# Performance work log

Hardware: AMD Instinct MI355X
Metric: run time of the kernel (lower is better)

Reference implementation:

```python
import jax, jax.numpy as jnp
import numpy as np
from jax.ops import segment_sum, segment_max

N = 20000   # nodes
E = 320000  # edges (no self loops; conv adds them)
G = 64      # graphs in batch
D = 128     # embed dim
H = 64      # GATConv out channels (heads=1)
L = 6       # number of conv/mlp blocks


def setup_inputs() -> dict:
    key = jax.random.key(0)
    ks = jax.random.split(key, 24)
    x_idx = jax.random.randint(ks[0], (N,), 0, 128)
    src = jax.random.randint(ks[1], (E,), 0, N)
    dst = jax.random.randint(ks[2], (E,), 0, N)
    dst = jnp.where(src == dst, (dst + 1) % N, dst)  # remove_self_loops semantics
    edge_index = jnp.stack([src, dst])
    edge_attr_idx = jax.random.randint(ks[3], (E,), 0, 128)
    batch = (jnp.arange(N) * G) // N  # sorted graph ids, ~312 nodes/graph
    s = 0.1
    r = lambda k, shp: jax.random.normal(k, shp, dtype=jnp.float32) * s
    return {
        'x_idx': x_idx, 'edge_index': edge_index, 'edge_attr_idx': edge_attr_idx, 'batch': batch,
        'emb': r(ks[4], (128, D)),
        'conv_W': r(ks[5], (L, D, H)), 'conv_We': r(ks[6], (L, D, H)),
        'conv_att_src': r(ks[7], (L, H)), 'conv_att_dst': r(ks[8], (L, H)),
        'conv_att_edge': r(ks[9], (L, H)), 'conv_b': jnp.zeros((L, H), jnp.float32),
        'mlp_W1': r(ks[10], (L, H, H)), 'mlp_b1': jnp.zeros((L, H), jnp.float32),
        'mlp_W2': r(ks[11], (L, H, H)), 'mlp_b2': jnp.zeros((L, H), jnp.float32),
        'mlp_W3': r(ks[12], (L, H, D)), 'mlp_b3': jnp.zeros((L, D), jnp.float32),
        'g1_W1': r(ks[13], (D, H)), 'g1_b1': jnp.zeros((H,), jnp.float32),
        'g1_W2': r(ks[14], (H, 1)), 'g1_b2': jnp.zeros((1,), jnp.float32),
        'g2_W1': r(ks[15], (D, H)), 'g2_b1': jnp.zeros((H,), jnp.float32),
        'g2_W2': r(ks[16], (H, D)), 'g2_b2': jnp.zeros((D,), jnp.float32),
        'p_W1': r(ks[17], (D, H)), 'p_b1': jnp.zeros((H,), jnp.float32),
        'p_W2': r(ks[18], (H, H)), 'p_b2': jnp.zeros((H,), jnp.float32),
        'p_W3': r(ks[19], (H, 1)), 'p_b3': jnp.zeros((1,), jnp.float32),
    }


def _mlp3(x, W1, b1, W2, b2, W3, b3):
    h = jax.nn.relu(x @ W1 + b1)
    h = jax.nn.relu(h @ W2 + b2)
    return h @ W3 + b3


def reference(x_idx, edge_index, edge_attr_idx, batch, emb, conv_W, conv_We,
              conv_att_src, conv_att_dst, conv_att_edge, conv_b,
              mlp_W1, mlp_b1, mlp_W2, mlp_b2, mlp_W3, mlp_b3,
              g1_W1, g1_b1, g1_W2, g1_b2, g2_W1, g2_b1, g2_W2, g2_b2,
              p_W1, p_b1, p_W2, p_b2, p_W3, p_b3):
    n = x_idx.shape[0]
    x = emb[x_idx]                 # [N,128]
    e = emb[edge_attr_idx]         # [E,128]
    src, dst = edge_index[0], edge_index[1]
    # add_self_loops with fill_value='mean': loop attr = mean of incoming edge attrs
    deg = segment_sum(jnp.ones((e.shape[0],), x.dtype), dst, num_segments=n)
    loop_attr = segment_sum(e, dst, num_segments=n) / jnp.maximum(deg, 1.0)[:, None]
    e_full = jnp.concatenate([e, loop_attr], axis=0)             # [E+N,128]
    ar = jnp.arange(n)
    src_f = jnp.concatenate([src, ar])
    dst_f = jnp.concatenate([dst, ar])

    def gat_conv(x, i):
        h = x @ conv_W[i]                       # [N,64]
        ep = e_full @ conv_We[i]                # [E+N,64]
        a_s = h @ conv_att_src[i]               # [N]
        a_d = h @ conv_att_dst[i]               # [N]
        a_e = ep @ conv_att_edge[i]             # [E+N]
        logit = jax.nn.leaky_relu(a_s[src_f] + a_d[dst_f] + a_e, 0.2)
        m = segment_max(logit, dst_f, num_segments=n)
        w = jnp.exp(logit - m[dst_f])
        denom = segment_sum(w, dst_f, num_segments=n)
        alpha = w / denom[dst_f]
        out = segment_sum(h[src_f] * alpha[:, None], dst_f, num_segments=n)
        return out + conv_b[i]

    jkn = []
    for i in range(L):  # dropout is identity at inference
        x = gat_conv(x, i)
        x = _mlp3(x, mlp_W1[i], mlp_b1[i], mlp_W2[i], mlp_b2[i], mlp_W3[i], mlp_b3[i])
        jkn.append(x)
    jkn = jnp.stack(jkn)                                  # [6,N,128]
    ms = jnp.sqrt(jnp.sum(jnp.square(jkn), axis=2))       # [6,N]
    ni = jnp.argmax(ms, axis=0)                           # [N]
    feature = jnp.take_along_axis(jkn, ni[None, :, None], axis=0)[0]  # [N,128]

    # per-graph attention pooling (vectorized over the per-graph loop)
    h1 = (jax.nn.relu(feature @ g1_W1 + g1_b1) @ g1_W2 + g1_b2)[:, 0]  # [N]
    m = segment_max(h1, batch, num_segments=G)
    w = jnp.exp(h1 - m[batch])
    attn = w / segment_sum(w, batch, num_segments=G)[batch]            # softmax per graph
    h2 = jax.nn.relu(feature @ g2_W1 + g2_b1) @ g2_W2 + g2_b2          # [N,128]
    counts = segment_sum(jnp.ones((n,), feature.dtype), batch, num_segments=G)
    hg = segment_sum(attn[:, None] * h2, batch, num_segments=G) / counts[:, None]  # [G,128]

    out = _mlp3(hg, p_W1, p_b1, p_W2, p_b2, p_W3, p_b3)   # [G,1]
    return out[:, 0]
```

## Files before the change

kernel.cpp:

```cpp
#include <hip/hip_runtime.h>
#include <math.h>

__device__ __forceinline__ float lrelu(float x){ return x > 0.0f ? x : 0.2f*x; }
__device__ __forceinline__ float bcastf(float v, int l){
    return __int_as_float(__builtin_amdgcn_readlane(__float_as_int(v), l));
}
__device__ __forceinline__ float wsum(float v){
    #pragma unroll
    for(int off=32; off; off>>=1) v += __shfl_xor(v, off, 64);
    return v;
}


__global__ void k_count(const int* __restrict__ dst, int* __restrict__ cnt, int E){
    int e = blockIdx.x*256 + threadIdx.x;
    if(e < E) atomicAdd(&cnt[dst[e]], 1);
}

__global__ __launch_bounds__(1024) void k_scan(const int* __restrict__ cnt, int* __restrict__ rowptr, int n){
    __shared__ int ws[16];
    __shared__ int carrysh;
    int t = threadIdx.x, lane = t & 63, wv = t >> 6;
    if(t==0){ carrysh = 0; rowptr[0] = 0; }
    __syncthreads();
    for(int base=0; base<n; base+=1024){
        int i = base + t;
        int v = (i<n) ? cnt[i] : 0;
        int s = v;
        #pragma unroll
        for(int off=1; off<64; off<<=1){ int u = __shfl_up(s, off, 64); if(lane>=off) s += u; }
        if(lane==63) ws[wv] = s;
        __syncthreads();
        if(t < 16){
            int u = ws[t];
            #pragma unroll
            for(int off=1; off<16; off<<=1){ int u2 = __shfl_up(u, off, 16); if(t>=off) u += u2; }
            ws[t] = u;
        }
        __syncthreads();
        int carry = carrysh;
        int wbase = wv ? ws[wv-1] : 0;
        if(i<n) rowptr[i+1] = carry + wbase + s;
        int total = ws[15];
        __syncthreads();
        if(t==0) carrysh = carry + total;
        __syncthreads();
    }
}

__global__ void k_scatter(const int* __restrict__ dst, const int* __restrict__ rowptr,
                          int* __restrict__ cnt2, int* __restrict__ eid, int E){
    int e = blockIdx.x*256 + threadIdx.x;
    if(e >= E) return;
    int d = dst[e];
    int p = rowptr[d] + atomicAdd(&cnt2[d], 1);
    eid[p] = e;
}

__global__ __launch_bounds__(256) void k_sortb(const int* __restrict__ rowptr, int* __restrict__ eid, int n){
    int node = blockIdx.x*4 + (threadIdx.x>>6);
    if(node >= n) return;
    int lane = threadIdx.x & 63;
    int b = rowptr[node], e = rowptr[node+1];
    int nj = e - b;
    if(nj <= 1) return;
    if(nj <= 64){
        int v = (lane < nj) ? eid[b+lane] : 0x7fffffff;
        for(int k=2; k<=64; k<<=1){
            for(int j=k>>1; j>0; j>>=1){
                int vv = __shfl_xor(v, j, 64);
                bool up = ((lane & k) == 0);
                bool lower = ((lane & j) == 0);
                int mn = min(v,vv), mx = max(v,vv);
                v = (lower == up) ? mn : mx;
            }
        }
        if(lane < nj) eid[b+lane] = v;
    } else if(lane == 0){
        for(int i=b+1; i<e; i++){
            int key = eid[i]; int j = i-1;
            while(j>=b && eid[j] > key){ eid[j+1] = eid[j]; j--; }
            eid[j+1] = key;
        }
    }
}

__global__ void k_pack(const int* __restrict__ eid, const int* __restrict__ src,
                       const int* __restrict__ eattr, int* __restrict__ packed, int E){
    int p = blockIdx.x*256 + threadIdx.x;
    if(p >= E) return;
    int e = eid[p];
    packed[p] = src[e] | (eattr[e] << 17);
}

__global__ __launch_bounds__(768) void k_table(const float* __restrict__ We, const float* __restrict__ atte,
                                               const float* __restrict__ emb, float* __restrict__ T){
    __shared__ float wv[768];
    int t = threadIdx.x;
    {
        int l = t>>7, k = t&127;
        const float* w = We + ((size_t)l*128 + k)*64;
        const float* a = atte + l*64;
        float s = 0.f;
        #pragma unroll 8
        for(int c=0;c<64;c++) s += w[c]*a[c];
        wv[t] = s;
    }
    __syncthreads();
    int l = t>>7, a = t&127;
    const float4* er = (const float4*)(emb + (size_t)a*128);
    const float* w = wv + l*128;
    float acc = 0.f;
    for(int k=0;k<32;k++){
        float4 v = er[k];
        acc += v.x*w[k*4+0] + v.y*w[k*4+1] + v.z*w[k*4+2] + v.w*w[k*4+3];
    }
    T[l*128 + a] = acc;
}


__global__ __launch_bounds__(256) void k_hx(const int* __restrict__ xidx, const float* __restrict__ emb,
        const float* __restrict__ W, const float* __restrict__ atts, const float* __restrict__ attd,
        float* __restrict__ h, float* __restrict__ as_, float* __restrict__ ad_, int n){
    int t = threadIdx.x, lane = t & 63;
    int base = blockIdx.x*16 + (t>>6)*4;
    if(base >= n) return;
    int nv = min(4, n - base);

    float xv0[4], xv1[4];
    #pragma unroll
    for(int nn=0;nn<4;nn++){
        if(nn < nv){
            int xi = xidx[base+nn];
            xv0[nn] = emb[(size_t)xi*128 + lane];
            xv1[nn] = emb[(size_t)xi*128 + 64 + lane];
        } else { xv0[nn]=0.f; xv1[nn]=0.f; }
    }
    float hv[4] = {0,0,0,0};
    #pragma unroll 8
    for(int k=0;k<64;k++){
        float w = W[k*64 + lane];
        #pragma unroll
        for(int nn=0;nn<4;nn++) hv[nn] = fmaf(bcastf(xv0[nn],k), w, hv[nn]);
    }
    #pragma unroll 8
    for(int k=0;k<64;k++){
        float w = W[(k+64)*64 + lane];
        #pragma unroll
        for(int nn=0;nn<4;nn++) hv[nn] = fmaf(bcastf(xv1[nn],k), w, hv[nn]);
    }
    float atl = atts[lane], adl = attd[lane];
    #pragma unroll
    for(int nn=0;nn<4;nn++){
        float sa = wsum(hv[nn]*atl);
        float sd = wsum(hv[nn]*adl);
        if(nn < nv){
            h[(size_t)(base+nn)*64 + lane] = hv[nn];
            if(lane==0){ as_[base+nn] = sa; ad_[base+nn] = sd; }
        }
    }
}


__global__ __launch_bounds__(256) void k_gat(const float* __restrict__ h,
        const float* __restrict__ as_, const float* __restrict__ ad_,
        const float* __restrict__ T, const int* __restrict__ packed,
        const int* __restrict__ rowptr, const float* __restrict__ bias,
        float* __restrict__ o, int n){
    __shared__ float Tl[128];
    if(threadIdx.x < 128) Tl[threadIdx.x] = T[threadIdx.x];
    __syncthreads();
    int node = blockIdx.x*4 + (threadIdx.x>>6);
    if(node >= n) return;
    int lane = threadIdx.x & 63;
    int b = rowptr[node], e = rowptr[node+1];
    float adv = ad_[node];
    float m = -1e30f, d = 0.f, sumae = 0.f;
    float a0=0.f, a1=0.f, a2=0.f, a3=0.f;
    for(int j0=b; j0<e; j0+=64){
        int nj = min(64, e-j0);
        int sj = 0; float aev = 0.f, lg = -1e30f;
        if(lane < nj){
            int pk = packed[j0+lane];
            sj  = pk & 0x1FFFF;
            aev = Tl[pk >> 17];
            lg  = lrelu(as_[sj] + adv + aev);
        }
        float cm = lg, sa = aev;
        #pragma unroll
        for(int off=32; off; off>>=1){ cm = fmaxf(cm, __shfl_xor(cm,off,64)); sa += __shfl_xor(sa,off,64); }
        sumae += sa;
        float nm = fmaxf(m, cm);
        float w = (lane<nj) ? expf(lg-nm) : 0.f;
        float ws = w;
        #pragma unroll
        for(int off=32; off; off>>=1) ws += __shfl_xor(ws,off,64);
        float scale = (m > -1e29f) ? expf(m-nm) : 0.f;
        d = d*scale + ws;
        a0*=scale; a1*=scale; a2*=scale; a3*=scale;
        int j = 0;
        for(; j+3<nj; j+=4){
            a0 = fmaf(bcastf(w,j+0), h[(size_t)__builtin_amdgcn_readlane(sj,j+0)*64 + lane], a0);
            a1 = fmaf(bcastf(w,j+1), h[(size_t)__builtin_amdgcn_readlane(sj,j+1)*64 + lane], a1);
            a2 = fmaf(bcastf(w,j+2), h[(size_t)__builtin_amdgcn_readlane(sj,j+2)*64 + lane], a2);
            a3 = fmaf(bcastf(w,j+3), h[(size_t)__builtin_amdgcn_readlane(sj,j+3)*64 + lane], a3);
        }
        for(; j<nj; j++)
            a0 = fmaf(bcastf(w,j), h[(size_t)__builtin_amdgcn_readlane(sj,j)*64 + lane], a0);
        m = nm;
    }
    int deg = e - b;
    float ael = sumae / fmaxf((float)deg, 1.f);
    float ls = lrelu(as_[node] + adv + ael);
    float nm = fmaxf(m, ls);
    float scale = (m > -1e29f) ? expf(m-nm) : 0.f;
    float wl = expf(ls-nm);
    d = d*scale + wl;
    float acc = (a0+a1)+(a2+a3);
    acc = acc*scale + wl*h[(size_t)node*64 + lane];
    o[(size_t)node*64 + lane] = acc/d + bias[lane];
}


__global__ __launch_bounds__(256) void k_dense(
    const float* __restrict__ o,
    const float* __restrict__ W1, const float* __restrict__ b1,
    const float* __restrict__ W2, const float* __restrict__ b2,
    const float* __restrict__ W3, const float* __restrict__ b3,
    float* __restrict__ bestF, float* __restrict__ bestMs, int layer,
    const float* __restrict__ Wn, const float* __restrict__ atts, const float* __restrict__ attd,
    float* __restrict__ hn, float* __restrict__ asn, float* __restrict__ adn_,
    const float* __restrict__ A, const float* __restrict__ g1b1,
    const float* __restrict__ w2, const float* __restrict__ g1b2,
    const float* __restrict__ B, const float* __restrict__ g2b1,
    const float* __restrict__ C, const float* __restrict__ g2b2,
    float* __restrict__ h1, float* __restrict__ h2,
    int n, int last)
{
    int t = threadIdx.x, lane = t & 63;
    int base = blockIdx.x*16 + (t>>6)*4;
    if(base >= n) return;
    int nv = min(4, n - base);

    float ov[4];
    #pragma unroll
    for(int nn=0;nn<4;nn++) ov[nn] = (nn<nv) ? o[(size_t)(base+nn)*64 + lane] : 0.f;

    float t1[4];
    {
        float bb = b1[lane];
        #pragma unroll
        for(int nn=0;nn<4;nn++) t1[nn] = bb;
        #pragma unroll 8
        for(int k=0;k<64;k++){
            float w = W1[k*64 + lane];
            #pragma unroll
            for(int nn=0;nn<4;nn++) t1[nn] = fmaf(bcastf(ov[nn],k), w, t1[nn]);
        }
        #pragma unroll
        for(int nn=0;nn<4;nn++) t1[nn] = fmaxf(t1[nn], 0.f);
    }

    float t2[4];
    {
        float bb = b2[lane];
        #pragma unroll
        for(int nn=0;nn<4;nn++) t2[nn] = bb;
        #pragma unroll 8
        for(int k=0;k<64;k++){
            float w = W2[k*64 + lane];
            #pragma unroll
            for(int nn=0;nn<4;nn++) t2[nn] = fmaf(bcastf(t1[nn],k), w, t2[nn]);
        }
        #pragma unroll
        for(int nn=0;nn<4;nn++) t2[nn] = fmaxf(t2[nn], 0.f);
    }

    float xp0[4], xp1[4];
    {
        float ba = b3[lane], bb = b3[lane+64];
        #pragma unroll
        for(int nn=0;nn<4;nn++){ xp0[nn]=ba; xp1[nn]=bb; }
        #pragma unroll 4
        for(int k=0;k<64;k++){
            float wa = W3[k*128 + lane];
            float wb = W3[k*128 + 64 + lane];
            #pragma unroll
            for(int nn=0;nn<4;nn++){
                float s = bcastf(t2[nn],k);
                xp0[nn] = fmaf(s, wa, xp0[nn]);
                xp1[nn] = fmaf(s, wb, xp1[nn]);
            }
        }
    }

    float msv[4]; bool upd[4];
    #pragma unroll
    for(int nn=0;nn<4;nn++){
        float p = wsum(xp0[nn]*xp0[nn] + xp1[nn]*xp1[nn]);
        msv[nn] = p;
        float prev = -1e30f;
        if(layer > 0 && nn < nv) prev = bestMs[base+nn];
        upd[nn] = (layer==0) || (p > prev);
    }

    if(!last){
        #pragma unroll
        for(int nn=0;nn<4;nn++){
            if(nn<nv && upd[nn]){
                bestF[(size_t)(base+nn)*128 + lane]      = xp0[nn];
                bestF[(size_t)(base+nn)*128 + 64 + lane] = xp1[nn];
                if(lane==0) bestMs[base+nn] = msv[nn];
            }
        }
        float hv[4] = {0,0,0,0};
        #pragma unroll 8
        for(int k=0;k<64;k++){
            float w = Wn[k*64 + lane];
            #pragma unroll
            for(int nn=0;nn<4;nn++) hv[nn] = fmaf(bcastf(xp0[nn],k), w, hv[nn]);
        }
        #pragma unroll 8
        for(int k=0;k<64;k++){
            float w = Wn[(k+64)*64 + lane];
            #pragma unroll
            for(int nn=0;nn<4;nn++) hv[nn] = fmaf(bcastf(xp1[nn],k), w, hv[nn]);
        }
        float atl = atts[lane], adl = attd[lane];
        #pragma unroll
        for(int nn=0;nn<4;nn++){
            float sa = wsum(hv[nn]*atl);
            float sd = wsum(hv[nn]*adl);
            if(nn<nv){
                hn[(size_t)(base+nn)*64 + lane] = hv[nn];
                if(lane==0){ asn[base+nn] = sa; adn_[base+nn] = sd; }
            }
        }
        return;
    }

    #pragma unroll
    for(int nn=0;nn<4;nn++){
        if(nn<nv && !upd[nn]){
            xp0[nn] = bestF[(size_t)(base+nn)*128 + lane];
            xp1[nn] = bestF[(size_t)(base+nn)*128 + 64 + lane];
        }
    }
    {
        float p1[4];
        float bb = g1b1[lane];
        #pragma unroll
        for(int nn=0;nn<4;nn++) p1[nn] = bb;
        #pragma unroll 8
        for(int k=0;k<64;k++){
            float w = A[k*64 + lane];
            #pragma unroll
            for(int nn=0;nn<4;nn++) p1[nn] = fmaf(bcastf(xp0[nn],k), w, p1[nn]);
        }
        #pragma unroll 8
        for(int k=0;k<64;k++){
            float w = A[(k+64)*64 + lane];
            #pragma unroll
            for(int nn=0;nn<4;nn++) p1[nn] = fmaf(bcastf(xp1[nn],k), w, p1[nn]);
        }
        float w2l = w2[lane], bout = g1b2[0];
        #pragma unroll
        for(int nn=0;nn<4;nn++){
            float s = wsum(fmaxf(p1[nn],0.f)*w2l);
            if(nn<nv && lane==0) h1[base+nn] = s + bout;
        }
    }
    float p2[4];
    {
        float bb = g2b1[lane];
        #pragma unroll
        for(int nn=0;nn<4;nn++) p2[nn] = bb;
        #pragma unroll 8
        for(int k=0;k<64;k++){
            float w = B[k*64 + lane];
            #pragma unroll
            for(int nn=0;nn<4;nn++) p2[nn] = fmaf(bcastf(xp0[nn],k), w, p2[nn]);
        }
        #pragma unroll 8
        for(int k=0;k<64;k++){
            float w = B[(k+64)*64 + lane];
            #pragma unroll
            for(int nn=0;nn<4;nn++) p2[nn] = fmaf(bcastf(xp1[nn],k), w, p2[nn]);
        }
        #pragma unroll
        for(int nn=0;nn<4;nn++) p2[nn] = fmaxf(p2[nn], 0.f);
    }
    {
        float r0[4], r1[4];
        float ba = g2b2[lane], bb = g2b2[lane+64];
        #pragma unroll
        for(int nn=0;nn<4;nn++){ r0[nn]=ba; r1[nn]=bb; }
        #pragma unroll 4
        for(int k=0;k<64;k++){
            float wa = C[k*128 + lane];
            float wb = C[k*128 + 64 + lane];
            #pragma unroll
            for(int nn=0;nn<4;nn++){
                float s = bcastf(p2[nn],k);
                r0[nn] = fmaf(s, wa, r0[nn]);
                r1[nn] = fmaf(s, wb, r1[nn]);
            }
        }
        #pragma unroll
        for(int nn=0;nn<4;nn++){
            if(nn<nv){
                h2[(size_t)(base+nn)*128 + lane]      = r0[nn];
                h2[(size_t)(base+nn)*128 + 64 + lane] = r1[nn];
            }
        }
    }
}


__global__ __launch_bounds__(128) void k_pool2(const float* __restrict__ h1, const float* __restrict__ h2,
                      float* __restrict__ wbuf,
                      const float* __restrict__ pW1, const float* __restrict__ pb1,
                      const float* __restrict__ pW2, const float* __restrict__ pb2,
                      const float* __restrict__ pW3, const float* __restrict__ pb3,
                      float* __restrict__ out, int n, int G){
    __shared__ float sh[128];
    __shared__ float hgrow[128];
    int g = blockIdx.x, tid = threadIdx.x;
    int start = (g*n + G-1)/G, end = ((g+1)*n + G-1)/G;
    float lm = -1e30f;
    for(int i=start+tid; i<end; i+=128) lm = fmaxf(lm, h1[i]);
    sh[tid]=lm; __syncthreads();
    for(int off=64; off; off>>=1){ if(tid<off) sh[tid]=fmaxf(sh[tid],sh[tid+off]); __syncthreads(); }
    float m = sh[0]; __syncthreads();
    float lsum = 0.f;
    for(int i=start+tid; i<end; i+=128){ float w = expf(h1[i]-m); wbuf[i]=w; lsum+=w; }
    sh[tid]=lsum; __syncthreads();
    for(int off=64; off; off>>=1){ if(tid<off) sh[tid]+=sh[tid+off]; __syncthreads(); }
    float denom = sh[0];
    float a0=0.f,a1=0.f,a2=0.f,a3=0.f;
    int i = start;
    for(; i+3<end; i+=4){
        a0 = fmaf(wbuf[i+0], h2[(size_t)(i+0)*128 + tid], a0);
        a1 = fmaf(wbuf[i+1], h2[(size_t)(i+1)*128 + tid], a1);
        a2 = fmaf(wbuf[i+2], h2[(size_t)(i+2)*128 + tid], a2);
        a3 = fmaf(wbuf[i+3], h2[(size_t)(i+3)*128 + tid], a3);
    }
    for(; i<end; i++) a0 = fmaf(wbuf[i], h2[(size_t)i*128 + tid], a0);
    float acc = (a0+a1)+(a2+a3);
    hgrow[tid] = acc/denom/(float)(end-start);
    __syncthreads();
    if(tid < 64){
        float t1v = pb1[tid];
        for(int k=0;k<128;k++) t1v = fmaf(hgrow[k], pW1[k*64+tid], t1v);
        t1v = fmaxf(t1v, 0.f);
        float t2v = pb2[tid];
        for(int k=0;k<64;k++) t2v = fmaf(__shfl(t1v,k,64), pW2[k*64+tid], t2v);
        t2v = fmaxf(t2v, 0.f);
        float s = t2v * pW3[tid];
        #pragma unroll
        for(int off=32; off; off>>=1) s += __shfl_xor(s,off,64);
        if(tid==0) out[g] = s + pb3[0];
    }
}

extern "C" void kernel_launch(void* const* d_in, const int* in_sizes, int n_in,
                              void* d_out, int out_size, void* d_ws, size_t ws_size,
                              hipStream_t stream){
    const int*   x_idx   = (const int*)  d_in[0];
    const int*   eindex  = (const int*)  d_in[1];
    const int*   eattr   = (const int*)  d_in[2];
    const float* emb     = (const float*)d_in[4];
    const float* conv_W  = (const float*)d_in[5];
    const float* conv_We = (const float*)d_in[6];
    const float* att_src = (const float*)d_in[7];
    const float* att_dst = (const float*)d_in[8];
    const float* att_edg = (const float*)d_in[9];
    const float* conv_b  = (const float*)d_in[10];
    const float* mW1 = (const float*)d_in[11]; const float* mb1 = (const float*)d_in[12];
    const float* mW2 = (const float*)d_in[13]; const float* mb2 = (const float*)d_in[14];
    const float* mW3 = (const float*)d_in[15]; const float* mb3 = (const float*)d_in[16];
    const float* g1W1= (const float*)d_in[17]; const float* g1b1= (const float*)d_in[18];
    const float* g1W2= (const float*)d_in[19]; const float* g1b2= (const float*)d_in[20];
    const float* g2W1= (const float*)d_in[21]; const float* g2b1= (const float*)d_in[22];
    const float* g2W2= (const float*)d_in[23]; const float* g2b2= (const float*)d_in[24];
    const float* pW1 = (const float*)d_in[25]; const float* pb1 = (const float*)d_in[26];
    const float* pW2 = (const float*)d_in[27]; const float* pb2 = (const float*)d_in[28];
    const float* pW3 = (const float*)d_in[29]; const float* pb3 = (const float*)d_in[30];

    const int N = in_sizes[0];
    const int E = in_sizes[2];
    const int G = out_size;
    const int* src = eindex;
    const int* dst = eindex + E;
    const int NW = (N + 3) / 4;
    const int ND = (N + 15) / 16;

    char* p = (char*)d_ws;
    auto alloc = [&](size_t bytes)->void*{ void* r = (void*)p; p += (bytes + 255) & ~(size_t)255; return r; };
    float* h      = (float*)alloc((size_t)N*64*4);
    float* o      = (float*)alloc((size_t)N*64*4);
    float* bestF  = (float*)alloc((size_t)N*128*4);
    float* h2buf  = (float*)alloc((size_t)N*128*4);
    float* bestMs = (float*)alloc((size_t)N*4);
    float* as_    = (float*)alloc((size_t)N*4);
    float* ad_    = (float*)alloc((size_t)N*4);
    float* Tbuf   = (float*)alloc(6*128*4);
    float* h1     = (float*)alloc((size_t)N*4);
    int*   cnt    = (int*)  alloc((size_t)N*4);
    int*   cnt2   = (int*)  alloc((size_t)N*4);
    int*   rowptr = (int*)  alloc((size_t)(N+1)*4);
    int*   eid    = (int*)  alloc((size_t)E*4);
    int*   packed = (int*)  alloc((size_t)E*4);

    hipMemsetAsync(cnt,  0, (size_t)N*4, stream);
    hipMemsetAsync(cnt2, 0, (size_t)N*4, stream);

    k_count<<<(E+255)/256, 256, 0, stream>>>(dst, cnt, E);
    k_scan<<<1, 1024, 0, stream>>>(cnt, rowptr, N);
    k_scatter<<<(E+255)/256, 256, 0, stream>>>(dst, rowptr, cnt2, eid, E);
    k_sortb<<<NW, 256, 0, stream>>>(rowptr, eid, N);
    k_pack<<<(E+255)/256, 256, 0, stream>>>(eid, src, eattr, packed, E);
    k_table<<<1, 768, 0, stream>>>(conv_We, att_edg, emb, Tbuf);
    k_hx<<<ND, 256, 0, stream>>>(x_idx, emb, conv_W, att_src, att_dst, h, as_, ad_, N);

    for(int l=0; l<6; l++){
        int last = (l==5) ? 1 : 0;
        const float* Wn   = last ? conv_W  : conv_W  + (size_t)(l+1)*8192;
        const float* atsn = last ? att_src : att_src + (l+1)*64;
        const float* atdn = last ? att_dst : att_dst + (l+1)*64;
        k_gat<<<NW, 256, 0, stream>>>(h, as_, ad_, Tbuf + l*128, packed, rowptr, conv_b + l*64, o, N);
        k_dense<<<ND, 256, 0, stream>>>(o,
            mW1 + (size_t)l*4096, mb1 + l*64, mW2 + (size_t)l*4096, mb2 + l*64,
            mW3 + (size_t)l*8192, mb3 + l*128,
            bestF, bestMs, l,
            Wn, atsn, atdn,
            h, as_, ad_,
            g1W1, g1b1, g1W2, g1b2, g2W1, g2b1, g2W2, g2b2,
            h1, h2buf,
            N, last);
    }

    k_pool2<<<G, 128, 0, stream>>>(h1, h2buf, bestMs,
            pW1, pb1, pW2, pb2, pW3, pb3, (float*)d_out, N, G);
}
```

Before: 530.9 us.

## Split each wave into half-wave node groups with vectorized loads and swizzle broadcasts

Rewrites the dense per-node MLP and projection kernels so that each wave processes four nodes as two 32-lane halves. Each half-wave owns two nodes, each lane holds 2 or 4 output columns, and loads are vectorized as float2/float4. Input values are broadcast with ds_swizzle inside 32-lane groups instead of readlane, using fully compile-time-unrolled loops. The intent is to cut scalar readlane traffic and the number of weight loads per FMA. The risks are heavy unrolling and register pressure, and swizzle goes through the LDS crossbar, which may add latency.

```diff
diff --git a/kernel.cpp b/kernel.cpp
--- a/kernel.cpp
+++ b/kernel.cpp
@@ -1,13 +1,33 @@
 #include <hip/hip_runtime.h>
 #include <math.h>
+#include <utility>
 
 __device__ __forceinline__ float lrelu(float x){ return x > 0.0f ? x : 0.2f*x; }
 __device__ __forceinline__ float bcastf(float v, int l){
     return __int_as_float(__builtin_amdgcn_readlane(__float_as_int(v), l));
 }
-__device__ __forceinline__ float wsum(float v){
+template<int J>
+__device__ __forceinline__ float swzbc(float v){
+    return __int_as_float(__builtin_amdgcn_ds_swizzle(__float_as_int(v), (J<<5)));
+}
+template<int C> __device__ __forceinline__ float getc4(const float4& v){
+    if constexpr(C==0) return v.x; else if constexpr(C==1) return v.y;
+    else if constexpr(C==2) return v.z; else return v.w;
+}
+template<int C> __device__ __forceinline__ float getc2(const float2& v){
+    if constexpr(C==0) return v.x; else return v.y;
+}
+template<class F, int... Is>
+__device__ __forceinline__ void unroll_impl(F&& f, std::integer_sequence<int, Is...>){
+    (f(std::integral_constant<int, Is>{}), ...);
+}
+template<int N, class F>
+__device__ __forceinline__ void unrollN(F&& f){
+    unroll_impl(static_cast<F&&>(f), std::make_integer_sequence<int, N>{});
+}
+__device__ __forceinline__ float hsum32(float v){
     #pragma unroll
-    for(int off=32; off; off>>=1) v += __shfl_xor(v, off, 64);
+    for(int off=16; off; off>>=1) v += __shfl_xor(v, off, 64);
     return v;
 }
 
@@ -125,40 +145,30 @@
     int t = threadIdx.x, lane = t & 63;
     int base = blockIdx.x*16 + (t>>6)*4;
     if(base >= n) return;
-    int nv = min(4, n - base);
-
-    float xv0[4], xv1[4];
-    #pragma unroll
-    for(int nn=0;nn<4;nn++){
-        if(nn < nv){
-            int xi = xidx[base+nn];
-            xv0[nn] = emb[(size_t)xi*128 + lane];
-            xv1[nn] = emb[(size_t)xi*128 + 64 + lane];
-        } else { xv0[nn]=0.f; xv1[nn]=0.f; }
-    }
-    float hv[4] = {0,0,0,0};
-    #pragma unroll 8
-    for(int k=0;k<64;k++){
-        float w = W[k*64 + lane];
-        #pragma unroll
-        for(int nn=0;nn<4;nn++) hv[nn] = fmaf(bcastf(xv0[nn],k), w, hv[nn]);
-    }
-    #pragma unroll 8
-    for(int k=0;k<64;k++){
-        float w = W[(k+64)*64 + lane];
-        #pragma unroll
-        for(int nn=0;nn<4;nn++) hv[nn] = fmaf(bcastf(xv1[nn],k), w, hv[nn]);
-    }
-    float atl = atts[lane], adl = attd[lane];
-    #pragma unroll
-    for(int nn=0;nn<4;nn++){
-        float sa = wsum(hv[nn]*atl);
-        float sd = wsum(hv[nn]*adl);
-        if(nn < nv){
-            h[(size_t)(base+nn)*64 + lane] = hv[nn];
-            if(lane==0){ as_[base+nn] = sa; ad_[base+nn] = sd; }
-        }
-    }
+    int cl = lane & 31, g = lane >> 5;
+    int ga = base + g*2, gb = ga + 1;
+    bool va = (ga < n), vb = (gb < n);
+
+    float4 x0 = va ? *(const float4*)(emb + (size_t)xidx[ga]*128 + 4*cl) : make_float4(0,0,0,0);
+    float4 x1 = vb ? *(const float4*)(emb + (size_t)xidx[gb]*128 + 4*cl) : make_float4(0,0,0,0);
+
+    float2 h0 = make_float2(0,0), h1v = make_float2(0,0);
+    unrollN<128>([&](auto kc){
+        constexpr int k = kc.value;
+        float2 w = *(const float2*)(W + k*64 + 2*cl);
+        float a0 = swzbc<(k>>2)>( getc4<(k&3)>(x0) );
+        float a1 = swzbc<(k>>2)>( getc4<(k&3)>(x1) );
+        h0.x  = fmaf(a0, w.x, h0.x);  h0.y  = fmaf(a0, w.y, h0.y);
+        h1v.x = fmaf(a1, w.x, h1v.x); h1v.y = fmaf(a1, w.y, h1v.y);
+    });
+    float2 ats = *(const float2*)(atts + 2*cl);
+    float2 atd = *(const float2*)(attd + 2*cl);
+    float pa0 = hsum32(h0.x*ats.x + h0.y*ats.y);
+    float pd0 = hsum32(h0.x*atd.x + h0.y*atd.y);
+    float pa1 = hsum32(h1v.x*ats.x + h1v.y*ats.y);
+    float pd1 = hsum32(h1v.x*atd.x + h1v.y*atd.y);
+    if(va){ *(float2*)(h + (size_t)ga*64 + 2*cl) = h0;  if(cl==0){ as_[ga]=pa0; ad_[ga]=pd0; } }
+    if(vb){ *(float2*)(h + (size_t)gb*64 + 2*cl) = h1v; if(cl==0){ as_[gb]=pa1; ad_[gb]=pd1; } }
 }
 
 
@@ -240,179 +250,127 @@
     int t = threadIdx.x, lane = t & 63;
     int base = blockIdx.x*16 + (t>>6)*4;
     if(base >= n) return;
-    int nv = min(4, n - base);
-
-    float ov[4];
-    #pragma unroll
-    for(int nn=0;nn<4;nn++) ov[nn] = (nn<nv) ? o[(size_t)(base+nn)*64 + lane] : 0.f;
-
-    float t1[4];
+    int cl = lane & 31, g = lane >> 5;
+    int ga = base + g*2, gb = ga + 1;
+    bool va = (ga < n), vb = (gb < n);
+
+    float2 o0 = va ? *(const float2*)(o + (size_t)ga*64 + 2*cl) : make_float2(0,0);
+    float2 o1 = vb ? *(const float2*)(o + (size_t)gb*64 + 2*cl) : make_float2(0,0);
+
+    float2 bv1 = *(const float2*)(b1 + 2*cl);
+    float2 t10 = bv1, t11 = bv1;
+    unrollN<64>([&](auto kc){
+        constexpr int k = kc.value;
+        float2 w = *(const float2*)(W1 + k*64 + 2*cl);
+        float a0 = swzbc<(k>>1)>( getc2<(k&1)>(o0) );
+        float a1 = swzbc<(k>>1)>( getc2<(k&1)>(o1) );
+        t10.x = fmaf(a0, w.x, t10.x); t10.y = fmaf(a0, w.y, t10.y);
+        t11.x = fmaf(a1, w.x, t11.x); t11.y = fmaf(a1, w.y, t11.y);
+    });
+    t10.x=fmaxf(t10.x,0.f); t10.y=fmaxf(t10.y,0.f);
+    t11.x=fmaxf(t11.x,0.f); t11.y=fmaxf(t11.y,0.f);
+
+    float2 bv2 = *(const float2*)(b2 + 2*cl);
+    float2 t20 = bv2, t21 = bv2;
+    unrollN<64>([&](auto kc){
+        constexpr int k = kc.value;
+        float2 w = *(const float2*)(W2 + k*64 + 2*cl);
+        float a0 = swzbc<(k>>1)>( getc2<(k&1)>(t10) );
+        float a1 = swzbc<(k>>1)>( getc2<(k&1)>(t11) );
+        t20.x = fmaf(a0, w.x, t20.x); t20.y = fmaf(a0, w.y, t20.y);
+        t21.x = fmaf(a1, w.x, t21.x); t21.y = fmaf(a1, w.y, t21.y);
+    });
+    t20.x=fmaxf(t20.x,0.f); t20.y=fmaxf(t20.y,0.f);
+    t21.x=fmaxf(t21.x,0.f); t21.y=fmaxf(t21.y,0.f);
+
+    float4 bq3 = *(const float4*)(b3 + 4*cl);
+    float4 x0 = bq3, x1 = bq3;
+    unrollN<64>([&](auto kc){
+        constexpr int k = kc.value;
+        float4 w = *(const float4*)(W3 + k*128 + 4*cl);
+        float a0 = swzbc<(k>>1)>( getc2<(k&1)>(t20) );
+        float a1 = swzbc<(k>>1)>( getc2<(k&1)>(t21) );
+        x0.x=fmaf(a0,w.x,x0.x); x0.y=fmaf(a0,w.y,x0.y); x0.z=fmaf(a0,w.z,x0.z); x0.w=fmaf(a0,w.w,x0.w);
+        x1.x=fmaf(a1,w.x,x1.x); x1.y=fmaf(a1,w.y,x1.y); x1.z=fmaf(a1,w.z,x1.z); x1.w=fmaf(a1,w.w,x1.w);
+    });
+
+    float ms0 = hsum32(x0.x*x0.x + x0.y*x0.y + x0.z*x0.z + x0.w*x0.w);
+    float ms1 = hsum32(x1.x*x1.x + x1.y*x1.y + x1.z*x1.z + x1.w*x1.w);
+    bool up0 = true, up1 = true;
+    if(layer > 0){
+        up0 = ms0 > (va ? bestMs[ga] : -1e30f);
+        up1 = ms1 > (vb ? bestMs[gb] : -1e30f);
+    }
+
+    if(!last){
+        if(va && up0){ *(float4*)(bestF + (size_t)ga*128 + 4*cl) = x0; if(cl==0) bestMs[ga] = ms0; }
+        if(vb && up1){ *(float4*)(bestF + (size_t)gb*128 + 4*cl) = x1; if(cl==0) bestMs[gb] = ms1; }
+        float2 h0 = make_float2(0,0), h1v = make_float2(0,0);
+        unrollN<128>([&](auto kc){
+            constexpr int k = kc.value;
+            float2 w = *(const float2*)(Wn + k*64 + 2*cl);
+            float a0 = swzbc<(k>>2)>( getc4<(k&3)>(x0) );
+            float a1 = swzbc<(k>>2)>( getc4<(k&3)>(x1) );
+            h0.x  = fmaf(a0, w.x, h0.x);  h0.y  = fmaf(a0, w.y, h0.y);
+            h1v.x = fmaf(a1, w.x, h1v.x); h1v.y = fmaf(a1, w.y, h1v.y);
+        });
+        float2 ats = *(const float2*)(atts + 2*cl);
+        float2 atd = *(const float2*)(attd + 2*cl);
+        float pa0 = hsum32(h0.x*ats.x + h0.y*ats.y);
+        float pd0 = hsum32(h0.x*atd.x + h0.y*atd.y);
+        float pa1 = hsum32(h1v.x*ats.x + h1v.y*ats.y);
+        float pd1 = hsum32(h1v.x*atd.x + h1v.y*atd.y);
+        if(va){ *(float2*)(hn + (size_t)ga*64 + 2*cl) = h0;  if(cl==0){ asn[ga]=pa0; adn_[ga]=pd0; } }
+        if(vb){ *(float2*)(hn + (size_t)gb*64 + 2*cl) = h1v; if(cl==0){ asn[gb]=pa1; adn_[gb]=pd1; } }
+        return;
+    }
+
+    if(va && !up0) x0 = *(const float4*)(bestF + (size_t)ga*128 + 4*cl);
+    if(vb && !up1) x1 = *(const float4*)(bestF + (size_t)gb*128 + 4*cl);
+
     {
-        float bb = b1[lane];
-        #pragma unroll
-        for(int nn=0;nn<4;nn++) t1[nn] = bb;
-        #pragma unroll 8
-        for(int k=0;k<64;k++){
-            float w = W1[k*64 + lane];
-            #pragma unroll
-            for(int nn=0;nn<4;nn++) t1[nn] = fmaf(bcastf(ov[nn],k), w, t1[nn]);
-        }
-        #pragma unroll
-        for(int nn=0;nn<4;nn++) t1[nn] = fmaxf(t1[nn], 0.f);
-    }
-
-    float t2[4];
+        float2 bg = *(const float2*)(g1b1 + 2*cl);
+        float2 p10 = bg, p11 = bg;
+        unrollN<128>([&](auto kc){
+            constexpr int k = kc.value;
+            float2 w = *(const float2*)(A + k*64 + 2*cl);
+            float a0 = swzbc<(k>>2)>( getc4<(k&3)>(x0) );
+            float a1 = swzbc<(k>>2)>( getc4<(k&3)>(x1) );
+            p10.x = fmaf(a0, w.x, p10.x); p10.y = fmaf(a0, w.y, p10.y);
+            p11.x = fmaf(a1, w.x, p11.x); p11.y = fmaf(a1, w.y, p11.y);
+        });
+        float2 w2v = *(const float2*)(w2 + 2*cl);
+        float s0 = hsum32(fmaxf(p10.x,0.f)*w2v.x + fmaxf(p10.y,0.f)*w2v.y);
+        float s1 = hsum32(fmaxf(p11.x,0.f)*w2v.x + fmaxf(p11.y,0.f)*w2v.y);
+        float bout = g1b2[0];
+        if(va && cl==0) h1[ga] = s0 + bout;
+        if(vb && cl==0) h1[gb] = s1 + bout;
+    }
+    float2 bg2 = *(const float2*)(g2b1 + 2*cl);
+    float2 p20 = bg2, p21 = bg2;
+    unrollN<128>([&](auto kc){
+        constexpr int k = kc.value;
+        float2 w = *(const float2*)(B + k*64 + 2*cl);
+        float a0 = swzbc<(k>>2)>( getc4<(k&3)>(x0) );
+        float a1 = swzbc<(k>>2)>( getc4<(k&3)>(x1) );
+        p20.x = fmaf(a0, w.x, p20.x); p20.y = fmaf(a0, w.y, p20.y);
+        p21.x = fmaf(a1, w.x, p21.x); p21.y = fmaf(a1, w.y, p21.y);
+    });
+    p20.x=fmaxf(p20.x,0.f); p20.y=fmaxf(p20.y,0.f);
+    p21.x=fmaxf(p21.x,0.f); p21.y=fmaxf(p21.y,0.f);
     {
-        float bb = b2[lane];
-        #pragma unroll
-        for(int nn=0;nn<4;nn++) t2[nn] = bb;
-        #pragma unroll 8
-        for(int k=0;k<64;k++){
-            float w = W2[k*64 + lane];
-            #pragma unroll
-            for(int nn=0;nn<4;nn++) t2[nn] = fmaf(bcastf(t1[nn],k), w, t2[nn]);
-        }
-        #pragma unroll
-        for(int nn=0;nn<4;nn++) t2[nn] = fmaxf(t2[nn], 0.f);
-    }
-
-    float xp0[4], xp1[4];
-    {
-        float ba = b3[lane], bb = b3[lane+64];
-        #pragma unroll
-        for(int nn=0;nn<4;nn++){ xp0[nn]=ba; xp1[nn]=bb; }
-        #pragma unroll 4
-        for(int k=0;k<64;k++){
-            float wa = W3[k*128 + lane];
-            float wb = W3[k*128 + 64 + lane];
-            #pragma unroll
-            for(int nn=0;nn<4;nn++){
-                float s = bcastf(t2[nn],k);
-                xp0[nn] = fmaf(s, wa, xp0[nn]);
-                xp1[nn] = fmaf(s, wb, xp1[nn]);
-            }
-        }
-    }
-
-    float msv[4]; bool upd[4];
-    #pragma unroll
-    for(int nn=0;nn<4;nn++){
-        float p = wsum(xp0[nn]*xp0[nn] + xp1[nn]*xp1[nn]);
-        msv[nn] = p;
-        float prev = -1e30f;
-        if(layer > 0 && nn < nv) prev = bestMs[base+nn];
-        upd[nn] = (layer==0) || (p > prev);
-    }
-
-    if(!last){
-        #pragma unroll
-        for(int nn=0;nn<4;nn++){
-            if(nn<nv && upd[nn]){
-                bestF[(size_t)(base+nn)*128 + lane]      = xp0[nn];
-                bestF[(size_t)(base+nn)*128 + 64 + lane] = xp1[nn];
-                if(lane==0) bestMs[base+nn] = msv[nn];
-            }
-        }
-        float hv[4] = {0,0,0,0};
-        #pragma unroll 8
-        for(int k=0;k<64;k++){
-            float w = Wn[k*64 + lane];
-            #pragma unroll
-            for(int nn=0;nn<4;nn++) hv[nn] = fmaf(bcastf(xp0[nn],k), w, hv[nn]);
-        }
-        #pragma unroll 8
-        for(int k=0;k<64;k++){
-            float w = Wn[(k+64)*64 + lane];
-            #pragma unroll
-            for(int nn=0;nn<4;nn++) hv[nn] = fmaf(bcastf(xp1[nn],k), w, hv[nn]);
-        }
-        float atl = atts[lane], adl = attd[lane];
-        #pragma unroll
-        for(int nn=0;nn<4;nn++){
-            float sa = wsum(hv[nn]*atl);
-            float sd = wsum(hv[nn]*adl);
-            if(nn<nv){
-                hn[(size_t)(base+nn)*64 + lane] = hv[nn];
-                if(lane==0){ asn[base+nn] = sa; adn_[base+nn] = sd; }
-            }
-        }
-        return;
-    }
-
-    #pragma unroll
-    for(int nn=0;nn<4;nn++){
-        if(nn<nv && !upd[nn]){
-            xp0[nn] = bestF[(size_t)(base+nn)*128 + lane];
-            xp1[nn] = bestF[(size_t)(base+nn)*128 + 64 + lane];
-        }
-    }
-    {
-        float p1[4];
-        float bb = g1b1[lane];
-        #pragma unroll
-        for(int nn=0;nn<4;nn++) p1[nn] = bb;
-        #pragma unroll 8
-        for(int k=0;k<64;k++){
-            float w = A[k*64 + lane];
-            #pragma unroll
-            for(int nn=0;nn<4;nn++) p1[nn] = fmaf(bcastf(xp0[nn],k), w, p1[nn]);
-        }
-        #pragma unroll 8
-        for(int k=0;k<64;k++){
-            float w = A[(k+64)*64 + lane];
-            #pragma unroll
-            for(int nn=0;nn<4;nn++) p1[nn] = fmaf(bcastf(xp1[nn],k), w, p1[nn]);
-        }
-        float w2l = w2[lane], bout = g1b2[0];
-        #pragma unroll
-        for(int nn=0;nn<4;nn++){
-            float s = wsum(fmaxf(p1[nn],0.f)*w2l);
-            if(nn<nv && lane==0) h1[base+nn] = s + bout;
-        }
-    }
-    float p2[4];
-    {
-        float bb = g2b1[lane];
-        #pragma unroll
-        for(int nn=0;nn<4;nn++) p2[nn] = bb;
-        #pragma unroll 8
-        for(int k=0;k<64;k++){
-            float w = B[k*64 + lane];
-            #pragma unroll
-            for(int nn=0;nn<4;nn++) p2[nn] = fmaf(bcastf(xp0[nn],k), w, p2[nn]);
-        }
-        #pragma unroll 8
-        for(int k=0;k<64;k++){
-            float w = B[(k+64)*64 + lane];
-            #pragma unroll
-            for(int nn=0;nn<4;nn++) p2[nn] = fmaf(bcastf(xp1[nn],k), w, p2[nn]);
-        }
-        #pragma unroll
-        for(int nn=0;nn<4;nn++) p2[nn] = fmaxf(p2[nn], 0.f);
-    }
-    {
-        float r0[4], r1[4];
-        float ba = g2b2[lane], bb = g2b2[lane+64];
-        #pragma unroll
-        for(int nn=0;nn<4;nn++){ r0[nn]=ba; r1[nn]=bb; }
-        #pragma unroll 4
-        for(int k=0;k<64;k++){
-            float wa = C[k*128 + lane];
-            float wb = C[k*128 + 64 + lane];
-            #pragma unroll
-            for(int nn=0;nn<4;nn++){
-                float s = bcastf(p2[nn],k);
-                r0[nn] = fmaf(s, wa, r0[nn]);
-                r1[nn] = fmaf(s, wb, r1[nn]);
-            }
-        }
-        #pragma unroll
-        for(int nn=0;nn<4;nn++){
-            if(nn<nv){
-                h2[(size_t)(base+nn)*128 + lane]      = r0[nn];
-                h2[(size_t)(base+nn)*128 + 64 + lane] = r1[nn];
-            }
-        }
+        float4 bq = *(const float4*)(g2b2 + 4*cl);
+        float4 r0 = bq, r1 = bq;
+        unrollN<64>([&](auto kc){
+            constexpr int k = kc.value;
+            float4 w = *(const float4*)(C + k*128 + 4*cl);
+            float a0 = swzbc<(k>>1)>( getc2<(k&1)>(p20) );
+            float a1 = swzbc<(k>>1)>( getc2<(k&1)>(p21) );
+            r0.x=fmaf(a0,w.x,r0.x); r0.y=fmaf(a0,w.y,r0.y); r0.z=fmaf(a0,w.z,r0.z); r0.w=fmaf(a0,w.w,r0.w);
+            r1.x=fmaf(a1,w.x,r1.x); r1.y=fmaf(a1,w.y,r1.y); r1.z=fmaf(a1,w.z,r1.z); r1.w=fmaf(a1,w.w,r1.w);
+        });
+        if(va) *(float4*)(h2 + (size_t)ga*128 + 4*cl) = r0;
+        if(vb) *(float4*)(h2 + (size_t)gb*128 + 4*cl) = r1;
     }
 }
 
```

Result: slower. 645.8 us (+21.6%).
